# Optimization experiments

Hardware: AMD Instinct MI355X
Metric: run time of the kernel (lower is better)

## Reference

```python
import jax, jax.numpy as jnp
import numpy as np

B, C, W, H = 16, 512, 64, 64
D = 16  # linear out features


def setup_inputs() -> dict:
    key = jax.random.key(0)
    k1, k2, k3, k4, k5 = jax.random.split(key, 5)
    x = jax.random.normal(k1, (B, C, W, H), dtype=jnp.float32)
    # nn.LazyLinear(16) with in_features = W*H
    Wq = jax.random.normal(k2, (D, W * H), dtype=jnp.float32) * 0.02
    bq = jnp.zeros((D,), dtype=jnp.float32)
    Wk = jax.random.normal(k3, (D, W * H), dtype=jnp.float32) * 0.02
    bk = jnp.zeros((D,), dtype=jnp.float32)
    return {"x": x, "Wq": Wq, "bq": bq, "Wk": Wk, "bk": bk}


def reference(x, Wq, bq, Wk, bk):
    b, c, w, h = x.shape
    xf = x.reshape(b, c, w * h)                      # [B, C, W*H]
    q = jnp.einsum('bcs,ds->bcd', xf, Wq) + bq       # [B, C, 16]
    k = jnp.einsum('bcs,ds->bcd', xf, Wk) + bk       # [B, C, 16]
    kq = jnp.einsum('bcd,bed->bce', q, k)            # [B, C, C]
    # torch nn.Softmax2d applies softmax over dim -3; for the 3D tensor
    # [B, C, C] that is the batch axis (axis 0) -- faithful reproduction.
    A = jax.nn.softmax(kq, axis=0)                   # [B, C, C]
    # Per-sample 1x1 conv with weight[o, i] = A[b, i, o] (note the transpose
    # from the permute([3,2,1,0]) in the torch code).
    out = jnp.einsum('bio,biwh->bowh', A, x)         # [B, C, W, H]
    return out
```

## Files before the change

kernel.cpp:

```cpp
#include <hip/hip_runtime.h>
#include <hip/hip_bf16.h>
#include <stdint.h>

typedef __attribute__((ext_vector_type(8))) short short8;
typedef __attribute__((ext_vector_type(4))) float floatx4;

#define B_ 16
#define C_ 512
#define S_ 4096
#define D_ 16

__device__ __forceinline__ unsigned short f2bf(float f) {
    union { float f; unsigned int i; } v;
    v.f = f;
    unsigned int u = v.i;
    return (unsigned short)((u + 0x7FFFu + ((u >> 16) & 1u)) >> 16);
}
__device__ __forceinline__ unsigned int pack2bf(float lo, float hi) {
    __hip_bfloat162 h = __float22bfloat162_rn(make_float2(lo, hi));
    union { __hip_bfloat162 h; unsigned int u; } v;
    v.h = h;
    return v.u;
}
__device__ __forceinline__ short8 cvt8p(float4 a, float4 b) {
    union { unsigned int u[4]; short8 s; } r;
    r.u[0] = pack2bf(a.x, a.y);
    r.u[1] = pack2bf(a.z, a.w);
    r.u[2] = pack2bf(b.x, b.y);
    r.u[3] = pack2bf(b.z, b.w);
    return r.s;
}

__device__ __forceinline__ void gl16(const void* g, void* l) {
    __builtin_amdgcn_global_load_lds(
        (const __attribute__((address_space(1))) unsigned int*)g,
        (__attribute__((address_space(3))) unsigned int*)l, 16, 0, 0);
}

template <int NS>
__global__ __launch_bounds__(256) void qk_kernel(
    const float* __restrict__ x,
    const float* __restrict__ Wq,
    const float* __restrict__ bq,
    const float* __restrict__ Wk,
    const float* __restrict__ bk,
    float* __restrict__ qkp)
{
    int lane = threadIdx.x & 63;
    int w    = threadIdx.x >> 6;
    int gw   = blockIdx.x * 4 + w;
    int row_tile = gw / NS;
    int ks       = gw % NS;
    int m  = lane & 15;
    int q8 = lane >> 4;
    int k0 = ks * (S_ / NS);

    const float* ax = x  + (size_t)(row_tile * 16 + m) * S_ + k0 + q8 * 8;
    const float* aq = Wq + (size_t)m * S_ + k0 + q8 * 8;
    const float* ak = Wk + (size_t)m * S_ + k0 + q8 * 8;

    floatx4 accq = {0.f, 0.f, 0.f, 0.f};
    floatx4 acck = {0.f, 0.f, 0.f, 0.f};
#pragma unroll 4
    for (int it = 0; it < S_ / NS / 32; ++it) {
        float4 xa = *(const float4*)(ax + it * 32);
        float4 xb2 = *(const float4*)(ax + it * 32 + 4);
        float4 qa = *(const float4*)(aq + it * 32);
        float4 qb = *(const float4*)(aq + it * 32 + 4);
        float4 ka = *(const float4*)(ak + it * 32);
        float4 kb2 = *(const float4*)(ak + it * 32 + 4);
        short8 a   = cvt8p(xa, xb2);
        short8 bq8 = cvt8p(qa, qb);
        short8 bk8 = cvt8p(ka, kb2);
        accq = __builtin_amdgcn_mfma_f32_16x16x32_bf16(a, bq8, accq, 0, 0, 0);
        acck = __builtin_amdgcn_mfma_f32_16x16x32_bf16(a, bk8, acck, 0, 0, 0);
    }
    float biasq = (ks == 0) ? bq[m] : 0.f;
    float biask = (ks == 0) ? bk[m] : 0.f;
    float* outp = qkp + (size_t)ks * 8192 * 32;
#pragma unroll
    for (int r = 0; r < 4; ++r) {
        int row = row_tile * 16 + q8 * 4 + r;
        outp[(size_t)row * 32 + m]      = accq[r] + biasq;
        outp[(size_t)row * 32 + 16 + m] = acck[r] + biask;
    }
}

template <int NS>
__global__ __launch_bounds__(256) void reduce_kernel(
    const float* __restrict__ qkp, float* __restrict__ qred)
{
    int g = blockIdx.x * 256 + threadIdx.x;
    const float4* p = (const float4*)qkp + g;
    float4 r = p[0];
#pragma unroll
    for (int k = 1; k < NS; ++k) {
        float4 v = p[(size_t)k * 65536];
        r.x += v.x; r.y += v.y; r.z += v.z; r.w += v.w;
    }
    ((float4*)qred)[g] = r;
}

__global__ __launch_bounds__(512) void softmax_kernel(
    const float* __restrict__ qred,
    unsigned short* __restrict__ Abf)
{
    __shared__ float lq[B_][32][17];
    __shared__ float lk[B_][16][17];
    int i0 = blockIdx.x * 32;
    int o0 = blockIdx.y * 16;
    int tid = threadIdx.x;

    {
        int d = tid & 15, il = tid >> 4;
#pragma unroll
        for (int b = 0; b < 16; ++b)
            lq[b][il][d] = qred[(size_t)(b * C_ + i0 + il) * 32 + d];
    }
    if (tid < 256) {
        int d = tid & 15, ol = tid >> 4;
#pragma unroll
        for (int b = 0; b < 16; ++b)
            lk[b][ol][d] = qred[(size_t)(b * C_ + o0 + ol) * 32 + 16 + d];
    }
    __syncthreads();

    int i = tid & 31;
    int o = tid >> 5;
    float v[16];
#pragma unroll
    for (int b = 0; b < 16; ++b) {
        float s = 0.f;
#pragma unroll
        for (int d = 0; d < 16; ++d) s += lq[b][i][d] * lk[b][o][d];
        v[b] = s;
    }
    float mx = v[0];
#pragma unroll
    for (int b = 1; b < 16; ++b) mx = fmaxf(mx, v[b]);
    float sum = 0.f;
#pragma unroll
    for (int b = 0; b < 16; ++b) { v[b] = __expf(v[b] - mx); sum += v[b]; }
    float inv = 1.0f / sum;
#pragma unroll
    for (int b = 0; b < 16; ++b)
        Abf[(size_t)(b * C_ + o0 + o) * C_ + i0 + i] = f2bf(v[b] * inv);
}

#define XP 36

__global__ __launch_bounds__(512) void av_kernel(
    const unsigned short* __restrict__ Abf,
    const float* __restrict__ x,
    float* __restrict__ out)
{
    __shared__ unsigned int At[256 * 32];
    __shared__ unsigned int Xt[128 * XP];
    int b  = blockIdx.z;
    int o0 = blockIdx.y * 256;
    int s0 = blockIdx.x * 128;
    int tid  = threadIdx.x;
    int lane = tid & 63;
    int w    = tid >> 6;
    int wm = (w >> 1) * 64;
    int wn = (w & 1) * 64;
    int fm = lane & 15;
    int q8 = lane >> 4;

    floatx4 acc[4][4];
#pragma unroll
    for (int a = 0; a < 4; ++a)
#pragma unroll
        for (int c = 0; c < 4; ++c) acc[a][c] = (floatx4){0.f, 0.f, 0.f, 0.f};

    const unsigned short* Ab = Abf + (size_t)b * C_ * C_;
    const float* xb = x + (size_t)b * C_ * S_;

    int arow_l = lane >> 3;
    int acol   = ((lane & 7) ^ (arow_l & 7)) * 8;

    int xc    = (tid >> 3) & 31;
    int xip   = tid & 7;
    int xhalf = tid >> 8;

    for (int kb = 0; kb < 8; ++kb) {
        int i0 = kb * 64;
#pragma unroll
        for (int q = 0; q < 4; ++q) {
            const unsigned short* gp =
                Ab + (size_t)(o0 + w * 32 + q * 8 + arow_l) * C_ + i0 + acol;
            unsigned int* lp = At + (w * 32 + q * 8) * 32;
            gl16(gp, lp);
        }
#pragma unroll
        for (int r = 0; r < 2; ++r) {
            int ip = xhalf * 16 + r * 8 + xip;
            const float* x0 = xb + (size_t)(i0 + 2 * ip) * S_ + s0 + xc * 4;
            float4 va = *(const float4*)x0;
            float4 vb = *(const float4*)(x0 + S_);
            unsigned int* dst = &Xt[(xc * 4) * XP + ip];
            dst[0 * XP] = pack2bf(va.x, vb.x);
            dst[1 * XP] = pack2bf(va.y, vb.y);
            dst[2 * XP] = pack2bf(va.z, vb.z);
            dst[3 * XP] = pack2bf(va.w, vb.w);
        }
        __syncthreads();

#pragma unroll
        for (int kc = 0; kc < 2; ++kc) {
            short8 af[4], bfr[4];
#pragma unroll
            for (int t = 0; t < 4; ++t)
                af[t] = *(const short8*)(&At[(wm + t * 16 + fm) * 32 +
                                             (((kc * 4 + q8) ^ (fm & 7)) << 2)]);
#pragma unroll
            for (int t = 0; t < 4; ++t)
                bfr[t] = *(const short8*)(&Xt[(wn + t * 16 + fm) * XP + kc * 16 + q8 * 4]);
#pragma unroll
            for (int a = 0; a < 4; ++a)
#pragma unroll
                for (int c = 0; c < 4; ++c)
                    acc[a][c] = __builtin_amdgcn_mfma_f32_16x16x32_bf16(af[a], bfr[c], acc[a][c], 0, 0, 0);
        }
        __syncthreads();
    }

    float* ob = out + (size_t)b * C_ * S_;
#pragma unroll
    for (int a = 0; a < 4; ++a) {
        int orow = o0 + wm + a * 16 + q8 * 4;
#pragma unroll
        for (int c = 0; c < 4; ++c) {
            int sc = s0 + wn + c * 16 + fm;
#pragma unroll
            for (int r = 0; r < 4; ++r)
                ob[(size_t)(orow + r) * S_ + sc] = acc[a][c][r];
        }
    }
}

extern "C" void kernel_launch(void* const* d_in, const int* in_sizes, int n_in,
                              void* d_out, int out_size, void* d_ws, size_t ws_size,
                              hipStream_t stream) {
    const float* x  = (const float*)d_in[0];
    const float* Wq = (const float*)d_in[1];
    const float* bq = (const float*)d_in[2];
    const float* Wk = (const float*)d_in[3];
    const float* bk = (const float*)d_in[4];
    float* out = (float*)d_out;

    if (ws_size >= (size_t)17 * 1024 * 1024) {
        float* qkp = (float*)d_ws;
        float* qred = (float*)((char*)d_ws + (size_t)8 * 1024 * 1024);
        unsigned short* Abf =
            (unsigned short*)((char*)d_ws + (size_t)9 * 1024 * 1024);
        qk_kernel<8><<<1024, 256, 0, stream>>>(x, Wq, bq, Wk, bk, qkp);
        reduce_kernel<8><<<256, 256, 0, stream>>>(qkp, qred);
        softmax_kernel<<<dim3(16, 32), 512, 0, stream>>>(qred, Abf);
        av_kernel<<<dim3(32, 2, 16), 512, 0, stream>>>(Abf, x, out);
    } else {
        float* qkp = (float*)d_ws;
        float* qred = (float*)((char*)d_ws + (size_t)4 * 1024 * 1024);
        unsigned short* Abf =
            (unsigned short*)((char*)d_ws + (size_t)5 * 1024 * 1024);
        qk_kernel<4><<<512, 256, 0, stream>>>(x, Wq, bq, Wk, bk, qkp);
        reduce_kernel<4><<<256, 256, 0, stream>>>(qkp, qred);
        softmax_kernel<<<dim3(16, 32), 512, 0, stream>>>(qred, Abf);
        av_kernel<<<dim3(32, 2, 16), 512, 0, stream>>>(Abf, x, out);
    }
}
```

Before: 308.2 us.

## Fold split-K reduction into softmax and register-prefetch x tiles in AV kernel

Removes the separate reduce kernel: the softmax kernel now sums the NS=8 split-K partials of q and k directly while loading them into shared memory, saving one launch and one round trip through global memory. The AV kernel also prefetches the next x tile into registers before the MFMA loop, so global load latency overlaps with compute. In exchange, each softmax block re-reads the partials redundantly, register pressure rises in av_kernel, and the small-workspace fallback path is dropped.

```diff
diff --git a/kernel.cpp b/kernel.cpp
--- a/kernel.cpp
+++ b/kernel.cpp
@@ -37,7 +37,8 @@
         (__attribute__((address_space(3))) unsigned int*)l, 16, 0, 0);
 }
 
-template <int NS>
+#define NS 8
+
 __global__ __launch_bounds__(256) void qk_kernel(
     const float* __restrict__ x,
     const float* __restrict__ Wq,
@@ -86,23 +87,8 @@
     }
 }
 
-template <int NS>
-__global__ __launch_bounds__(256) void reduce_kernel(
-    const float* __restrict__ qkp, float* __restrict__ qred)
-{
-    int g = blockIdx.x * 256 + threadIdx.x;
-    const float4* p = (const float4*)qkp + g;
-    float4 r = p[0];
-#pragma unroll
-    for (int k = 1; k < NS; ++k) {
-        float4 v = p[(size_t)k * 65536];
-        r.x += v.x; r.y += v.y; r.z += v.z; r.w += v.w;
-    }
-    ((float4*)qred)[g] = r;
-}
-
 __global__ __launch_bounds__(512) void softmax_kernel(
-    const float* __restrict__ qred,
+    const float* __restrict__ qkp,
     unsigned short* __restrict__ Abf)
 {
     __shared__ float lq[B_][32][17];
@@ -113,15 +99,27 @@
 
     {
         int d = tid & 15, il = tid >> 4;
-#pragma unroll
-        for (int b = 0; b < 16; ++b)
-            lq[b][il][d] = qred[(size_t)(b * C_ + i0 + il) * 32 + d];
+#pragma unroll 4
+        for (int b = 0; b < 16; ++b) {
+            size_t base = (size_t)(b * C_ + i0 + il) * 32 + d;
+            float s = 0.f;
+#pragma unroll 4
+            for (int ks = 0; ks < NS; ++ks)
+                s += qkp[(size_t)ks * 8192 * 32 + base];
+            lq[b][il][d] = s;
+        }
     }
     if (tid < 256) {
         int d = tid & 15, ol = tid >> 4;
-#pragma unroll
-        for (int b = 0; b < 16; ++b)
-            lk[b][ol][d] = qred[(size_t)(b * C_ + o0 + ol) * 32 + 16 + d];
+#pragma unroll 4
+        for (int b = 0; b < 16; ++b) {
+            size_t base = (size_t)(b * C_ + o0 + ol) * 32 + 16 + d;
+            float s = 0.f;
+#pragma unroll 4
+            for (int ks = 0; ks < NS; ++ks)
+                s += qkp[(size_t)ks * 8192 * 32 + base];
+            lk[b][ol][d] = s;
+        }
     }
     __syncthreads();
 
@@ -183,6 +181,15 @@
     int xip   = tid & 7;
     int xhalf = tid >> 8;
 
+    float4 xva[2], xvb[2];
+#pragma unroll
+    for (int r = 0; r < 2; ++r) {
+        int ip = xhalf * 16 + r * 8 + xip;
+        const float* x0 = xb + (size_t)(2 * ip) * S_ + s0 + xc * 4;
+        xva[r] = *(const float4*)x0;
+        xvb[r] = *(const float4*)(x0 + S_);
+    }
+
     for (int kb = 0; kb < 8; ++kb) {
         int i0 = kb * 64;
 #pragma unroll
@@ -195,16 +202,24 @@
 #pragma unroll
         for (int r = 0; r < 2; ++r) {
             int ip = xhalf * 16 + r * 8 + xip;
-            const float* x0 = xb + (size_t)(i0 + 2 * ip) * S_ + s0 + xc * 4;
-            float4 va = *(const float4*)x0;
-            float4 vb = *(const float4*)(x0 + S_);
             unsigned int* dst = &Xt[(xc * 4) * XP + ip];
-            dst[0 * XP] = pack2bf(va.x, vb.x);
-            dst[1 * XP] = pack2bf(va.y, vb.y);
-            dst[2 * XP] = pack2bf(va.z, vb.z);
-            dst[3 * XP] = pack2bf(va.w, vb.w);
+            dst[0 * XP] = pack2bf(xva[r].x, xvb[r].x);
+            dst[1 * XP] = pack2bf(xva[r].y, xvb[r].y);
+            dst[2 * XP] = pack2bf(xva[r].z, xvb[r].z);
+            dst[3 * XP] = pack2bf(xva[r].w, xvb[r].w);
         }
         __syncthreads();
+
+        if (kb + 1 < 8) {
+#pragma unroll
+            for (int r = 0; r < 2; ++r) {
+                int ip = xhalf * 16 + r * 8 + xip;
+                const float* x0 =
+                    xb + (size_t)((kb + 1) * 64 + 2 * ip) * S_ + s0 + xc * 4;
+                xva[r] = *(const float4*)x0;
+                xvb[r] = *(const float4*)(x0 + S_);
+            }
+        }
 
 #pragma unroll
         for (int kc = 0; kc < 2; ++kc) {
@@ -249,23 +264,11 @@
     const float* bk = (const float*)d_in[4];
     float* out = (float*)d_out;
 
-    if (ws_size >= (size_t)17 * 1024 * 1024) {
-        float* qkp = (float*)d_ws;
-        float* qred = (float*)((char*)d_ws + (size_t)8 * 1024 * 1024);
-        unsigned short* Abf =
-            (unsigned short*)((char*)d_ws + (size_t)9 * 1024 * 1024);
-        qk_kernel<8><<<1024, 256, 0, stream>>>(x, Wq, bq, Wk, bk, qkp);
-        reduce_kernel<8><<<256, 256, 0, stream>>>(qkp, qred);
-        softmax_kernel<<<dim3(16, 32), 512, 0, stream>>>(qred, Abf);
-        av_kernel<<<dim3(32, 2, 16), 512, 0, stream>>>(Abf, x, out);
-    } else {
-        float* qkp = (float*)d_ws;
-        float* qred = (float*)((char*)d_ws + (size_t)4 * 1024 * 1024);
-        unsigned short* Abf =
-            (unsigned short*)((char*)d_ws + (size_t)5 * 1024 * 1024);
-        qk_kernel<4><<<512, 256, 0, stream>>>(x, Wq, bq, Wk, bk, qkp);
-        reduce_kernel<4><<<256, 256, 0, stream>>>(qkp, qred);
-        softmax_kernel<<<dim3(16, 32), 512, 0, stream>>>(qred, Abf);
-        av_kernel<<<dim3(32, 2, 16), 512, 0, stream>>>(Abf, x, out);
-    }
-}
+    float* qkp = (float*)d_ws;
+    unsigned short* Abf =
+        (unsigned short*)((char*)d_ws + (size_t)8 * 1024 * 1024);
+
+    qk_kernel<<<1024, 256, 0, stream>>>(x, Wq, bq, Wk, bk, qkp);
+    softmax_kernel<<<dim3(16, 32), 512, 0, stream>>>(qkp, Abf);
+    av_kernel<<<dim3(32, 2, 16), 512, 0, stream>>>(Abf, x, out);
+}
```

Result: slower. 328.2 us (+6.5%).
